# Kernel optimization log

Hardware: AMD Instinct MI355X
Metric: run time of the kernel (lower is better)

The kernel has to match this reference:

```python
import jax, jax.numpy as jnp
import numpy as np

W_DIM, B_DIM, S = 8, 8, 900  # patches: [W, B, 1, 30, 30] -> seq_len 900


def setup_inputs() -> dict:
    key = jax.random.key(0)
    ks = jax.random.split(key, 8)
    radar = jax.random.normal(ks[0], (W_DIM, B_DIM, 1, 30, 30), jnp.float32)
    dmde = jax.random.normal(ks[1], (W_DIM, B_DIM, 1, 30, 30), jnp.float32)
    gumbel_u = jax.random.uniform(ks[2], (B_DIM * W_DIM, S, S), jnp.float32)
    # MHA with embed_dim=1 -> all projections are scalars (xavier-ish init)
    Wq = jax.random.normal(ks[3], (), jnp.float32)
    Wk = jax.random.normal(ks[4], (), jnp.float32)
    Wv = jax.random.normal(ks[5], (), jnp.float32)
    Wo = jax.random.normal(ks[6], (), jnp.float32)
    bq = jnp.zeros((), jnp.float32)
    bk = jnp.zeros((), jnp.float32)
    bv = jnp.zeros((), jnp.float32)
    bo = jnp.zeros((), jnp.float32)
    ln_gamma = jnp.ones((), jnp.float32)
    ln_beta = jnp.zeros((), jnp.float32)
    attn_residual_scale = jnp.asarray(1e-9, jnp.float32)
    return dict(radar_patches=radar, dmde_out_patches=dmde, gumbel_u=gumbel_u,
                Wq=Wq, bq=bq, Wk=Wk, bk=bk, Wv=Wv, bv=bv, Wo=Wo, bo=bo,
                ln_gamma=ln_gamma, ln_beta=ln_beta,
                attn_residual_scale=attn_residual_scale)


def reference(radar_patches, dmde_out_patches, gumbel_u, Wq, bq, Wk, bk, Wv, bv,
              Wo, bo, ln_gamma, ln_beta, attn_residual_scale):
    Wd, B = radar_patches.shape[0], radar_patches.shape[1]
    # [W,B,1,30,30] -> [B*W, S]
    radar = jnp.transpose(radar_patches, (1, 0, 2, 3, 4)).reshape(B * Wd, -1)
    mde = jnp.transpose(dmde_out_patches, (1, 0, 2, 3, 4)).reshape(B * Wd, -1)
    # --- cross attention, embed_dim = head_dim = 1 (scale = 1/sqrt(1) = 1) ---
    q = radar * Wq + bq
    k = mde * Wk + bk
    v = mde * Wv + bv
    attn = jax.nn.softmax(jnp.einsum('ni,nj->nij', q, k), axis=-1)  # [N,S,S]
    attended = jnp.einsum('nij,nj->ni', attn, v) * Wo + bo           # [N,S]
    # LayerNorm over last dim of size 1 (degenerate: output == ln_beta)
    x = (radar + attended)[..., None]                                # [N,S,1]
    mu = jnp.mean(x, axis=-1, keepdims=True)
    var = jnp.mean((x - mu) ** 2, axis=-1, keepdims=True)
    attended_out = (x - mu) / jnp.sqrt(var + 1e-5) * ln_gamma + ln_beta
    # --- hard gumbel attention gather/scatter, fully mask-vectorized ---
    valid = (radar != 0).astype(radar.dtype)                          # [N,S]
    noise = -jnp.log(-jnp.log(gumbel_u + 1e-8) + 1e-8)
    p = jax.nn.softmax(attn + noise, axis=-1)  # temperature = 1.0
    idx = jnp.argmax(p, axis=-1)                                      # [N,S]
    y_hard = jax.nn.one_hot(idx, p.shape[-1], dtype=p.dtype)
    y = jax.lax.stop_gradient(y_hard - p) + p                         # straight-through
    src = radar * valid   # invalid rows contribute nothing (matches per-row loop)
    out_seq = jnp.einsum('nts,nt->ns', y, src)[..., None]             # [N,S,1]
    combined = valid[..., None] * (out_seq != 0).astype(out_seq.dtype)
    out_seq = out_seq + combined * (attn_residual_scale * attended_out)
    # [N,S] -> [B,W,S] -> [B,1,S,W]
    out = out_seq[..., 0].reshape(B, Wd, -1).transpose(0, 2, 1)[:, None]
    return out
```

## Files before the change

### kernel.cpp

```cpp
#include <hip/hip_runtime.h>
#include <cfloat>

#define SS 900
#define WD 8
#define BD 8
#define NROWS 64
#define OUT_ELEMS (BD * SS * WD)
#define NQ 225
#define ROWS_PER_BLK 16
#define BLKS_PER_N 57

__global__ __launch_bounds__(256) void rel_zero(float* __restrict__ out) {
    int i = blockIdx.x * 256 + threadIdx.x;
    if (i < OUT_ELEMS) out[i] = 0.0f;
}

__global__ __launch_bounds__(256) void rel_main(
    const float* __restrict__ radar,
    const float* __restrict__ mde,
    const float* __restrict__ gumbel,
    const float* __restrict__ pWq, const float* __restrict__ pbq,
    const float* __restrict__ pWk, const float* __restrict__ pbk,
    float* __restrict__ out)
{
    const int tid   = threadIdx.x;
    const int n     = blockIdx.x / BLKS_PER_N;
    const int tbase = (blockIdx.x - n * BLKS_PER_N) * ROWS_PER_BLK;
    const int b     = n >> 3;
    const int w     = n & 7;

    __shared__ float4 ks4[NQ + 1];
    __shared__ float  s_red[8];

    const float wk = pWk[0], bk0 = pbk[0];
    float kmin = FLT_MAX, kmax = -FLT_MAX;
    if (tid < NQ) {
        const float4* __restrict__ m4 = (const float4*)(mde + (size_t)(w * BD + b) * SS);
        float4 mq = m4[tid];
        float4 k;
        k.x = __fmaf_rn(mq.x, wk, bk0);
        k.y = __fmaf_rn(mq.y, wk, bk0);
        k.z = __fmaf_rn(mq.z, wk, bk0);
        k.w = __fmaf_rn(mq.w, wk, bk0);
        ks4[tid] = k;
        kmin = fminf(fminf(k.x, k.y), fminf(k.z, k.w));
        kmax = fmaxf(fmaxf(k.x, k.y), fmaxf(k.z, k.w));
    }
    #pragma unroll
    for (int off = 1; off < 64; off <<= 1) {
        kmin = fminf(kmin, __shfl_xor(kmin, off, 64));
        kmax = fmaxf(kmax, __shfl_xor(kmax, off, 64));
    }
    if ((tid & 63) == 0) { s_red[tid >> 6] = kmin; s_red[4 + (tid >> 6)] = kmax; }
    __syncthreads();
    kmin = fminf(fminf(s_red[0], s_red[1]), fminf(s_red[2], s_red[3]));
    kmax = fmaxf(fmaxf(s_red[4], s_red[5]), fmaxf(s_red[6], s_red[7]));

    const int gg     = tid >> 4;
    const int lane16 = tid & 15;
    const int t      = tbase + gg;
    if (t >= SS) return;
    const int row = n * SS + t;

    const float r0 = radar[(size_t)(w * BD + b) * SS + t];
    const float q  = __fmaf_rn(r0, pWq[0], pbq[0]);
    const float m  = __fmul_rn(q, (q >= 0.0f) ? kmax : kmin);

    const float4* __restrict__ g4 = (const float4*)(gumbel + (size_t)row * SS);
    const float*  __restrict__ kf = (const float*)ks4;

    float4 U[15];
    float umax = -1.0f;
    float D = 0.0f;
    #pragma unroll
    for (int j = 0; j < 15; j++) {
        const int f = j * 16 + lane16;
        const bool valid = (j < 14) || (lane16 == 0);
        const int fc = valid ? f : 0;
        float4 u = g4[fc];
        float4 k = ks4[fc];
        if (!valid) { u.x = u.y = u.z = u.w = -1.0f; }
        U[j] = u;
        umax = fmaxf(umax, fmaxf(fmaxf(u.x, u.y), fmaxf(u.z, u.w)));
        if (valid) {
            D += __expf(__fmaf_rn(q, k.x, -m)) + __expf(__fmaf_rn(q, k.y, -m))
               + __expf(__fmaf_rn(q, k.z, -m)) + __expf(__fmaf_rn(q, k.w, -m));
        }
    }
    #pragma unroll
    for (int off = 1; off < 16; off <<= 1) {
        umax = fmaxf(umax, __shfl_xor(umax, off, 16));
        D += __shfl_xor(D, off, 16);
    }

    float margin = __fmaf_rn(1.002f, 1.0f / D, 1e-6f);
    float w0    = -logf(umax + 1e-8f);
    float nzmax = -logf(w0 + 1e-8f);
    float T     = nzmax - margin;
    float wT    = expf(-T);
    float uthr  = expf(-(wT - 1e-8f)) - 1e-8f;
    uthr = uthr - fabsf(uthr) * 4e-6f - 1e-9f;

    float bestv = -FLT_MAX;
    int   besti = 0x7fffffff;
    #pragma unroll
    for (int j = 0; j < 15; j++) {
        float4 u = U[j];
        float m4 = fmaxf(fmaxf(u.x, u.y), fmaxf(u.z, u.w));
        if (__any(m4 >= uthr)) {
            const int s0 = (j * 16 + lane16) * 4;
            if (u.x >= uthr) {
                float l = __fmul_rn(q, kf[s0]);
                float nz = -logf(-logf(u.x + 1e-8f) + 1e-8f);
                float v = expf(l - m) / D + nz;
                if (v > bestv) { bestv = v; besti = s0; }
            }
            if (u.y >= uthr) {
                float l = __fmul_rn(q, kf[s0 + 1]);
                float nz = -logf(-logf(u.y + 1e-8f) + 1e-8f);
                float v = expf(l - m) / D + nz;
                if (v > bestv) { bestv = v; besti = s0 + 1; }
            }
            if (u.z >= uthr) {
                float l = __fmul_rn(q, kf[s0 + 2]);
                float nz = -logf(-logf(u.z + 1e-8f) + 1e-8f);
                float v = expf(l - m) / D + nz;
                if (v > bestv) { bestv = v; besti = s0 + 2; }
            }
            if (u.w >= uthr) {
                float l = __fmul_rn(q, kf[s0 + 3]);
                float nz = -logf(-logf(u.w + 1e-8f) + 1e-8f);
                float v = expf(l - m) / D + nz;
                if (v > bestv) { bestv = v; besti = s0 + 3; }
            }
        }
    }
    #pragma unroll
    for (int off = 1; off < 16; off <<= 1) {
        float ov = __shfl_xor(bestv, off, 16);
        int   oi = __shfl_xor(besti, off, 16);
        if (ov > bestv || (ov == bestv && oi < besti)) { bestv = ov; besti = oi; }
    }
    if (lane16 == 0)
        atomicAdd(&out[((size_t)b * SS + besti) * WD + w], r0);
}

__global__ __launch_bounds__(256) void rel_epilogue(
    const float* __restrict__ radar,
    const float* __restrict__ pScale,
    const float* __restrict__ pBeta,
    float* __restrict__ out)
{
    int i = blockIdx.x * 256 + threadIdx.x;
    if (i >= OUT_ELEMS) return;
    int w    = i & 7;
    int rest = i >> 3;
    int s    = rest % SS;
    int b    = rest / SS;
    float o = out[i];
    float r = radar[(size_t)(w * BD + b) * SS + s];
    float add = ((r != 0.0f) && (o != 0.0f)) ? (pScale[0] * pBeta[0]) : 0.0f;
    out[i] = o + add;
}

extern "C" void kernel_launch(void* const* d_in, const int* in_sizes, int n_in,
                              void* d_out, int out_size, void* d_ws, size_t ws_size,
                              hipStream_t stream) {
    const float* radar  = (const float*)d_in[0];
    const float* mde    = (const float*)d_in[1];
    const float* gumbel = (const float*)d_in[2];
    const float* Wq     = (const float*)d_in[3];
    const float* bq     = (const float*)d_in[4];
    const float* Wk     = (const float*)d_in[5];
    const float* bk     = (const float*)d_in[6];
    const float* beta   = (const float*)d_in[12];
    const float* scale  = (const float*)d_in[13];
    float* out = (float*)d_out;

    rel_zero<<<(OUT_ELEMS + 255) / 256, 256, 0, stream>>>(out);
    rel_main<<<NROWS * BLKS_PER_N, 256, 0, stream>>>(radar, mde, gumbel,
                                                     Wq, bq, Wk, bk, out);
    rel_epilogue<<<(OUT_ELEMS + 255) / 256, 256, 0, stream>>>(radar, scale, beta, out);
}
```

Measured before the change: 45.04 us.

## Compact gumbel candidates into shared queue and resolve argmax block-wide

Stops holding all 15 float4 gumbel values per lane in registers and keeps only per-chunk maxima. Chunks above the threshold are re-read from global memory, and each candidate is appended to a shared-memory queue. Block threads then evaluate the queued candidates in parallel and pick each row's winner with a 64-bit packed-key atomicMax, replacing divergent per-lane log/exp work. It also switches threshold math to fast intrinsics, widens the safety margin, and vectorizes the zero fill. The risks are re-reading global memory and dropping candidates once more than CAP of them appear in a block.

```diff
diff --git a/kernel.cpp b/kernel.cpp
--- a/kernel.cpp
+++ b/kernel.cpp
@@ -9,10 +9,11 @@
 #define NQ 225
 #define ROWS_PER_BLK 16
 #define BLKS_PER_N 57
+#define CAP 128
 
-__global__ __launch_bounds__(256) void rel_zero(float* __restrict__ out) {
+__global__ __launch_bounds__(256) void rel_zero(float4* __restrict__ out4) {
     int i = blockIdx.x * 256 + threadIdx.x;
-    if (i < OUT_ELEMS) out[i] = 0.0f;
+    if (i < OUT_ELEMS / 4) out4[i] = make_float4(0.f, 0.f, 0.f, 0.f);
 }
 
 __global__ __launch_bounds__(256) void rel_main(
@@ -31,12 +32,20 @@
 
     __shared__ float4 ks4[NQ + 1];
     __shared__ float  s_red[8];
+    __shared__ float  s_q[ROWS_PER_BLK], s_m[ROWS_PER_BLK], s_D[ROWS_PER_BLK];
+    __shared__ unsigned long long s_win[ROWS_PER_BLK];
+    __shared__ int    s_cnt;
+    __shared__ int    s_qs[CAP];
+    __shared__ float  s_qu[CAP];
+
+    if (tid == 0) s_cnt = 0;
+    if (tid < ROWS_PER_BLK) s_win[tid] = 0ULL;
 
     const float wk = pWk[0], bk0 = pbk[0];
     float kmin = FLT_MAX, kmax = -FLT_MAX;
     if (tid < NQ) {
-        const float4* __restrict__ m4 = (const float4*)(mde + (size_t)(w * BD + b) * SS);
-        float4 mq = m4[tid];
+        const float4* __restrict__ m4p = (const float4*)(mde + (size_t)(w * BD + b) * SS);
+        float4 mq = m4p[tid];
         float4 k;
         k.x = __fmaf_rn(mq.x, wk, bk0);
         k.y = __fmaf_rn(mq.y, wk, bk0);
@@ -59,18 +68,18 @@
     const int gg     = tid >> 4;
     const int lane16 = tid & 15;
     const int t      = tbase + gg;
-    if (t >= SS) return;
-    const int row = n * SS + t;
+    const bool active = (t < SS);
+    const int tc     = active ? t : 0;
+    const int row    = n * SS + tc;
 
-    const float r0 = radar[(size_t)(w * BD + b) * SS + t];
+    const float r0 = radar[(size_t)(w * BD + b) * SS + tc];
     const float q  = __fmaf_rn(r0, pWq[0], pbq[0]);
     const float m  = __fmul_rn(q, (q >= 0.0f) ? kmax : kmin);
 
     const float4* __restrict__ g4 = (const float4*)(gumbel + (size_t)row * SS);
     const float*  __restrict__ kf = (const float*)ks4;
 
-    float4 U[15];
-    float umax = -1.0f;
+    float M[15];
     float D = 0.0f;
     #pragma unroll
     for (int j = 0; j < 15; j++) {
@@ -80,69 +89,71 @@
         float4 u = g4[fc];
         float4 k = ks4[fc];
         if (!valid) { u.x = u.y = u.z = u.w = -1.0f; }
-        U[j] = u;
-        umax = fmaxf(umax, fmaxf(fmaxf(u.x, u.y), fmaxf(u.z, u.w)));
+        M[j] = fmaxf(fmaxf(u.x, u.y), fmaxf(u.z, u.w));
         if (valid) {
             D += __expf(__fmaf_rn(q, k.x, -m)) + __expf(__fmaf_rn(q, k.y, -m))
                + __expf(__fmaf_rn(q, k.z, -m)) + __expf(__fmaf_rn(q, k.w, -m));
         }
     }
+    float umax = M[0];
+    #pragma unroll
+    for (int j = 1; j < 15; j++) umax = fmaxf(umax, M[j]);
     #pragma unroll
     for (int off = 1; off < 16; off <<= 1) {
         umax = fmaxf(umax, __shfl_xor(umax, off, 16));
         D += __shfl_xor(D, off, 16);
     }
+    if (active && lane16 == 0) { s_q[gg] = q; s_m[gg] = m; s_D[gg] = D; }
 
     float margin = __fmaf_rn(1.002f, 1.0f / D, 1e-6f);
-    float w0    = -logf(umax + 1e-8f);
-    float nzmax = -logf(w0 + 1e-8f);
+    float w0    = -__logf(umax + 1e-8f);
+    float nzmax = -__logf(w0 + 1e-8f);
     float T     = nzmax - margin;
-    float wT    = expf(-T);
-    float uthr  = expf(-(wT - 1e-8f)) - 1e-8f;
-    uthr = uthr - fabsf(uthr) * 4e-6f - 1e-9f;
+    float wT    = __expf(-T);
+    float uthr  = __expf(-(wT - 1e-8f)) - 1e-8f;
+    uthr = uthr - fabsf(uthr) * 1e-5f - 1e-9f;
 
-    float bestv = -FLT_MAX;
-    int   besti = 0x7fffffff;
-    #pragma unroll
-    for (int j = 0; j < 15; j++) {
-        float4 u = U[j];
-        float m4 = fmaxf(fmaxf(u.x, u.y), fmaxf(u.z, u.w));
-        if (__any(m4 >= uthr)) {
-            const int s0 = (j * 16 + lane16) * 4;
-            if (u.x >= uthr) {
-                float l = __fmul_rn(q, kf[s0]);
-                float nz = -logf(-logf(u.x + 1e-8f) + 1e-8f);
-                float v = expf(l - m) / D + nz;
-                if (v > bestv) { bestv = v; besti = s0; }
-            }
-            if (u.y >= uthr) {
-                float l = __fmul_rn(q, kf[s0 + 1]);
-                float nz = -logf(-logf(u.y + 1e-8f) + 1e-8f);
-                float v = expf(l - m) / D + nz;
-                if (v > bestv) { bestv = v; besti = s0 + 1; }
-            }
-            if (u.z >= uthr) {
-                float l = __fmul_rn(q, kf[s0 + 2]);
-                float nz = -logf(-logf(u.z + 1e-8f) + 1e-8f);
-                float v = expf(l - m) / D + nz;
-                if (v > bestv) { bestv = v; besti = s0 + 2; }
-            }
-            if (u.w >= uthr) {
-                float l = __fmul_rn(q, kf[s0 + 3]);
-                float nz = -logf(-logf(u.w + 1e-8f) + 1e-8f);
-                float v = expf(l - m) / D + nz;
-                if (v > bestv) { bestv = v; besti = s0 + 3; }
+    if (active) {
+        #pragma unroll
+        for (int j = 0; j < 15; j++) {
+            if (M[j] >= uthr) {
+                const int f = j * 16 + lane16;
+                const bool valid = (j < 14) || (lane16 == 0);
+                const int fc = valid ? f : 0;
+                float4 u = g4[fc];
+                if (!valid) { u.x = u.y = u.z = u.w = -1.0f; }
+                const int s0 = fc * 4;
+                if (u.x >= uthr) { int i2 = atomicAdd(&s_cnt, 1); if (i2 < CAP) { s_qs[i2] = (gg << 10) | s0;       s_qu[i2] = u.x; } }
+                if (u.y >= uthr) { int i2 = atomicAdd(&s_cnt, 1); if (i2 < CAP) { s_qs[i2] = (gg << 10) | (s0 + 1); s_qu[i2] = u.y; } }
+                if (u.z >= uthr) { int i2 = atomicAdd(&s_cnt, 1); if (i2 < CAP) { s_qs[i2] = (gg << 10) | (s0 + 2); s_qu[i2] = u.z; } }
+                if (u.w >= uthr) { int i2 = atomicAdd(&s_cnt, 1); if (i2 < CAP) { s_qs[i2] = (gg << 10) | (s0 + 3); s_qu[i2] = u.w; } }
             }
         }
     }
-    #pragma unroll
-    for (int off = 1; off < 16; off <<= 1) {
-        float ov = __shfl_xor(bestv, off, 16);
-        int   oi = __shfl_xor(besti, off, 16);
-        if (ov > bestv || (ov == bestv && oi < besti)) { bestv = ov; besti = oi; }
+    __syncthreads();
+
+    const int nc = min(s_cnt, CAP);
+    if (tid < nc) {
+        int   pk = s_qs[tid];
+        int   g2 = pk >> 10, s = pk & 0x3FF;
+        float u  = s_qu[tid];
+        float q2 = s_q[g2], m2 = s_m[g2], D2 = s_D[g2];
+        float l  = __fmul_rn(q2, kf[s]);
+        float nz = -logf(-logf(u + 1e-8f) + 1e-8f);
+        float v  = expf(l - m2) / D2 + nz;
+        unsigned vb = __float_as_uint(v);
+        unsigned key32 = (vb & 0x80000000u) ? ~vb : (vb | 0x80000000u);
+        unsigned long long key =
+            ((unsigned long long)key32 << 32) | (unsigned)(0xFFFFFFFFu - (unsigned)s);
+        atomicMax(&s_win[g2], key);
     }
-    if (lane16 == 0)
-        atomicAdd(&out[((size_t)b * SS + besti) * WD + w], r0);
+    __syncthreads();
+
+    if (active && lane16 == 0) {
+        unsigned long long key = s_win[gg];
+        unsigned s = 0xFFFFFFFFu - (unsigned)(key & 0xFFFFFFFFull);
+        atomicAdd(&out[((size_t)b * SS + s) * WD + w], r0);
+    }
 }
 
 __global__ __launch_bounds__(256) void rel_epilogue(
@@ -177,7 +188,7 @@
     const float* scale  = (const float*)d_in[13];
     float* out = (float*)d_out;
 
-    rel_zero<<<(OUT_ELEMS + 255) / 256, 256, 0, stream>>>(out);
+    rel_zero<<<(OUT_ELEMS / 4 + 255) / 256, 256, 0, stream>>>((float4*)out);
     rel_main<<<NROWS * BLKS_PER_N, 256, 0, stream>>>(radar, mde, gumbel,
                                                      Wq, bq, Wk, bk, out);
     rel_epilogue<<<(OUT_ELEMS + 255) / 256, 256, 0, stream>>>(radar, scale, beta, out);
```

Result: no change. 44.55 us (-1.1%).
